# Performance work log

Hardware: AMD Instinct MI355X
Metric: run time of the kernel (lower is better)

Reference implementation:

```python
import jax, jax.numpy as jnp
import numpy as np

P = 14  # chain length, hard-coded by edge_index construction (range(14))
B = 4096
BN_EPS = 1e-5
ALPHA = 1.0
DIMS = [(3, 64), (64, 64), (64, 64), (64, 128), (128, 1024)]


def setup_inputs() -> dict:
    key = jax.random.key(0)
    ks = jax.random.split(key, 40)
    inp = {}
    inp["x1"] = jax.random.normal(ks[0], (B, 3, P), jnp.float32)
    inp["x2"] = jax.random.normal(ks[1], (B, 3, P), jnp.float32)
    for li, (din, dout) in enumerate(DIMS, 1):
        inp[f"W{li}"] = jax.random.normal(ks[1 + li], (din, dout), jnp.float32) / np.float32(np.sqrt(din))
        inp[f"b{li}"] = jnp.zeros((dout,), jnp.float32)
        inp[f"gamma{li}"] = jnp.ones((dout,), jnp.float32)
        inp[f"beta{li}"] = jnp.zeros((dout,), jnp.float32)
    inp["emb_W"] = jax.random.normal(ks[10], (1024, 10), jnp.float32) / np.float32(32.0)
    inp["emb_b"] = jnp.zeros((10,), jnp.float32)
    inp["clu_W"] = jax.random.normal(ks[11], (800, 10), jnp.float32) * np.float32(0.1)  # xavier-ish
    return inp


def _chain_agg(h):
    # h: [B*P, d]; equivalent to A @ h where A is the block-diagonal chain
    # adjacency (i<->i+1, no self-loops) built by the original Python loop.
    h3 = h.reshape(B, P, -1)
    agg = (jnp.pad(h3[:, 1:], ((0, 0), (0, 1), (0, 0)))
           + jnp.pad(h3[:, :-1], ((0, 0), (1, 0), (0, 0))))
    return agg.reshape(B * P, -1)


def _gcn_block(h, W, b, gamma, beta):
    # GCNConv: A @ (X W) + b ; then BatchNorm1d (training stats) ; ReLU
    h = _chain_agg(h @ W) + b
    mu = h.mean(axis=0)
    var = ((h - mu) ** 2).mean(axis=0)  # biased var, as torch BN uses for normalization
    h = gamma * (h - mu) * jax.lax.rsqrt(var + BN_EPS) + beta
    return jax.nn.relu(h)


def _forward_single(x, params):
    # x: [B, 3, P] -> [B, P, 3] -> [B*P, 3]
    h = jnp.transpose(x, (0, 2, 1)).reshape(B * P, 3)
    for li in range(1, 6):
        h = _gcn_block(h, params[f"W{li}"], params[f"b{li}"], params[f"gamma{li}"], params[f"beta{li}"])
    h = h.reshape(B, P, -1).max(axis=1)            # [B, 1024]
    extra = h @ params["emb_W"] + params["emb_b"]  # [B, 10]
    # ClusterlingLayer (Student-t assignment)
    d = jnp.sum((extra[:, None, :] - params["clu_W"]) ** 2, axis=2)  # [B, 800]
    q = (1.0 + d / ALPHA) ** (-(ALPHA + 1.0) / 2.0)
    q = q / q.sum(axis=1, keepdims=True)
    return q, extra, d


def reference(x1, x2, W1, b1, gamma1, beta1, W2, b2, gamma2, beta2,
              W3, b3, gamma3, beta3, W4, b4, gamma4, beta4,
              W5, b5, gamma5, beta5, emb_W, emb_b, clu_W):
    params = dict(W1=W1, b1=b1, gamma1=gamma1, beta1=beta1,
                  W2=W2, b2=b2, gamma2=gamma2, beta2=beta2,
                  W3=W3, b3=b3, gamma3=gamma3, beta3=beta3,
                  W4=W4, b4=b4, gamma4=gamma4, beta4=beta4,
                  W5=W5, b5=b5, gamma5=gamma5, beta5=beta5,
                  emb_W=emb_W, emb_b=emb_b, clu_W=clu_W)
    c1, e1, d1 = _forward_single(x1, params)
    c2, e2, d2 = _forward_single(x2, params)
    sim = jnp.linalg.norm(e1 - e2 + 1e-6, axis=1)  # torch pairwise_distance eps
    return sim, c1, c2, e1, e2, d1
```

## Files before the change

kernel.cpp:

```cpp
#include <hip/hip_runtime.h>
#include <hip/hip_bf16.h>

#define NB 4096
#define PLEN 14
#define NROWS (NB*PLEN)
#define BN_EPS 1e-5f

#define SLOT_STRIDE 32768
#define INP_STRIDE  133120
#define SLOT5_OFF   131072
#define NBANK 16

typedef __bf16 bf16x8 __attribute__((ext_vector_type(8)));
typedef float  f32x4  __attribute__((ext_vector_type(4)));

__global__ __launch_bounds__(256) void wprep_kernel(
    const float* __restrict__ W2, const float* __restrict__ W3,
    const float* __restrict__ W4, const float* __restrict__ W5,
    __bf16* __restrict__ wt2, __bf16* __restrict__ wt3,
    __bf16* __restrict__ wt4, __bf16* __restrict__ wt5b,
    float* __restrict__ stats)
{
    int idx = blockIdx.x*256 + threadIdx.x;
    if (idx < 2*INP_STRIDE) { stats[idx] = 0.f; return; }
    idx -= 2*INP_STRIDE;
    if (idx < 4096) { int n = idx>>6, k = idx&63; wt2[idx] = (__bf16)W2[k*64+n]; return; }
    idx -= 4096;
    if (idx < 4096) { int n = idx>>6, k = idx&63; wt3[idx] = (__bf16)W3[k*64+n]; return; }
    idx -= 4096;
    if (idx < 8192) { int n = idx>>6, k = idx&63; wt4[idx] = (__bf16)W4[k*128+n]; return; }
    idx -= 8192;
    int kk = idx & 7, n = (idx >> 3) & 63, kg = (idx >> 9) & 15, c = idx >> 13;
    wt5b[idx] = (__bf16)W5[(kg*8 + kk)*1024 + c*64 + n];
}

__global__ __launch_bounds__(256) void l1_kernel(
    const float* __restrict__ x1,
    const float* __restrict__ x2,
    const float* __restrict__ W,
    const float* __restrict__ bias,
    __bf16* __restrict__ pre,
    float* __restrict__ stats)
{
    const int col  = threadIdx.x & 63;
    const int sub  = threadIdx.x >> 6;
    const int chain = blockIdx.x * 4 + sub;
    const int inp  = chain >> 12;
    const int bank = blockIdx.x & (NBANK-1);
    const float w0 = W[0*64+col], w1 = W[1*64+col], w2 = W[2*64+col];
    const float bb = bias[col];
    const float* xb = (inp ? x2 : x1) + (chain & 4095)*3*PLEN;
    float s = 0.f, s2 = 0.f;
    for (int p = 0; p < PLEN; p++) {
        float u0 = 0.f, u1 = 0.f, u2 = 0.f;
        if (p > 0)      { u0 += xb[p-1]; u1 += xb[PLEN+p-1]; u2 += xb[2*PLEN+p-1]; }
        if (p < PLEN-1) { u0 += xb[p+1]; u1 += xb[PLEN+p+1]; u2 += xb[2*PLEN+p+1]; }
        float v = u0*w0 + u1*w1 + u2*w2 + bb;
        pre[(size_t)(chain*PLEN + p)*64 + col] = (__bf16)v;
        s += v; s2 += v*v;
    }
    __shared__ float ss[4][64], ssq[4][64];
    ss[sub][col] = s; ssq[sub][col] = s2;
    __syncthreads();
    if (sub == 0) {
        float ts  = ss[0][col]+ss[1][col]+ss[2][col]+ss[3][col];
        float ts2 = ssq[0][col]+ssq[1][col]+ssq[2][col]+ssq[3][col];
        float* st = stats + inp*INP_STRIDE + bank*2048;
        atomicAdd(&st[col], ts);
        atomicAdd(&st[1024 + col], ts2);
    }
}

template<int NOUT>
__global__ __launch_bounds__(256) void layer_kernel(
    const __bf16* __restrict__ prev,
    const float* __restrict__ stats_in,
    const float* __restrict__ gamma, const float* __restrict__ beta,
    const __bf16* __restrict__ wt,
    const float* __restrict__ bias,
    __bf16* __restrict__ outp,
    float* __restrict__ stats_out)
{
    constexpr int KP = 72;
    constexpr int NCH = NOUT/64;
    __shared__ __align__(16) short sA[64*KP];
    const int tid = threadIdx.x, wave = tid >> 6, lane = tid & 63;
    const int m = lane & 15, q = lane >> 4;
    const int rowbase = blockIdx.x * 56;
    const int soff = (blockIdx.x >> 10) * INP_STRIDE;
    const int bank = blockIdx.x & (NBANK-1);
    const float* sin_ = stats_in + soff;

    bf16x8 breg[NCH][2];
    #pragma unroll
    for (int cc = 0; cc < NCH; ++cc)
        #pragma unroll
        for (int ksi = 0; ksi < 2; ++ksi)
            breg[cc][ksi] = *reinterpret_cast<const bf16x8*>(
                wt + (cc*64 + wave*16 + m)*64 + ksi*32 + q*8);

    #pragma unroll
    for (int i = tid; i < 512; i += 256) {
        int rr = 56 + (i >> 6), cc = i & 63;
        sA[rr*KP + cc] = 0;
    }
    {
        const int ch = tid >> 6, c = tid & 63;
        float sb = 0.f, qb = 0.f;
        #pragma unroll
        for (int bk = 0; bk < NBANK; ++bk) {
            sb += sin_[bk*2048 + c];
            qb += sin_[bk*2048 + 1024 + c];
        }
        float mu = sb*(1.f/NROWS);
        float vr = qb*(1.f/NROWS) - mu*mu;
        float a = gamma[c]*rsqrtf(vr+BN_EPS), c0 = beta[c]-mu*a;
        float h[14];
        const __bf16* src = prev + (size_t)(rowbase + ch*14)*64 + c;
        #pragma unroll
        for (int r = 0; r < 14; ++r)
            h[r] = fmaxf(a*(float)src[r*64] + c0, 0.f);
        #pragma unroll
        for (int r = 0; r < 14; ++r) {
            float g = (r>0 ? h[r-1] : 0.f) + (r<13 ? h[r+1] : 0.f);
            union { __bf16 b; short s; } pk;
            pk.b = (__bf16)g;
            sA[(ch*14+r)*KP + c] = pk.s;
        }
    }
    __syncthreads();

    f32x4 acc[NCH][4];
    #pragma unroll
    for (int cc = 0; cc < NCH; ++cc)
        #pragma unroll
        for (int t = 0; t < 4; ++t) acc[cc][t] = (f32x4){0.f,0.f,0.f,0.f};

    #pragma unroll
    for (int ksi = 0; ksi < 2; ++ksi) {
        bf16x8 af[4];
        #pragma unroll
        for (int t = 0; t < 4; ++t)
            af[t] = *reinterpret_cast<const bf16x8*>(&sA[(t*16+m)*KP + ksi*32 + q*8]);
        #pragma unroll
        for (int cc = 0; cc < NCH; ++cc)
            #pragma unroll
            for (int t = 0; t < 4; ++t)
                acc[cc][t] = __builtin_amdgcn_mfma_f32_16x16x32_bf16(af[t], breg[cc][ksi], acc[cc][t], 0, 0, 0);
    }

    float* stout = stats_out + soff + bank*2048;
    #pragma unroll
    for (int cc = 0; cc < NCH; ++cc) {
        const int ocol = cc*64 + wave*16 + m;
        const float bb = bias[ocol];
        float s = 0.f, s2 = 0.f;
        #pragma unroll
        for (int t = 0; t < 4; ++t) {
            if (t == 3 && q >= 2) continue;
            #pragma unroll
            for (int r = 0; r < 4; ++r) {
                float v = acc[cc][t][r] + bb;
                outp[(size_t)(rowbase + t*16 + q*4 + r)*NOUT + ocol] = (__bf16)v;
                s += v; s2 += v*v;
            }
        }
        s  += __shfl_xor(s, 16);  s  += __shfl_xor(s, 32);
        s2 += __shfl_xor(s2, 16); s2 += __shfl_xor(s2, 32);
        if (lane < 16) {
            atomicAdd(&stout[ocol], s);
            atomicAdd(&stout[1024 + ocol], s2);
        }
    }
}

__global__ __launch_bounds__(256, 1) void l5_kernel(
    const __bf16* __restrict__ prev,
    const float* __restrict__ stats_in,
    const float* __restrict__ gamma, const float* __restrict__ beta,
    const __bf16* __restrict__ wtb,
    const float* __restrict__ bias,
    const float* __restrict__ g5,
    __bf16* __restrict__ osel,
    float* __restrict__ part)
{
    __shared__ __align__(16) short sA[112*136];
    const int tid = threadIdx.x, wave = tid >> 6, lane = tid & 63;
    const int m = lane & 15, q = lane >> 4;
    const int rowbase = blockIdx.x * 112;
    const int soff = (blockIdx.x >> 9) * INP_STRIDE;
    const float* sin_ = stats_in + soff;
    float* pb = part + (size_t)blockIdx.x * 2048;

    const char* gw = (const char*)wtb;
    const int boffB = q*1024 + (wave*16 + m)*16;

    bf16x8 bA[4], bB[4];
    #pragma unroll
    for (int k4 = 0; k4 < 4; ++k4)
        bA[k4] = *reinterpret_cast<const bf16x8*>(gw + boffB + k4*4096);

    {
        const int ch = tid >> 5, c4 = (tid & 31)*4;
        float aa[4], cc4[4];
        #pragma unroll
        for (int j = 0; j < 4; ++j) {
            float sb = 0.f, qb = 0.f;
            #pragma unroll
            for (int bk = 0; bk < NBANK; ++bk) {
                sb += sin_[bk*2048 + c4+j];
                qb += sin_[bk*2048 + 1024 + c4+j];
            }
            float mu = sb*(1.f/NROWS);
            float vr = qb*(1.f/NROWS) - mu*mu;
            aa[j] = gamma[c4+j]*rsqrtf(vr+BN_EPS);
            cc4[j] = beta[c4+j] - mu*aa[j];
        }
        float h[14][4];
        const __bf16* src = prev + (size_t)(rowbase + ch*14)*128 + c4;
        #pragma unroll
        for (int r = 0; r < 14; ++r) {
            union { uint2 u; __bf16 b[4]; } ld;
            ld.u = *reinterpret_cast<const uint2*>(src + r*128);
            h[r][0] = fmaxf(aa[0]*(float)ld.b[0] + cc4[0], 0.f);
            h[r][1] = fmaxf(aa[1]*(float)ld.b[1] + cc4[1], 0.f);
            h[r][2] = fmaxf(aa[2]*(float)ld.b[2] + cc4[2], 0.f);
            h[r][3] = fmaxf(aa[3]*(float)ld.b[3] + cc4[3], 0.f);
        }
        const int qq = ch >> 1, jb = (ch & 1) * 14;
        #pragma unroll
        for (int p = 0; p < 14; ++p) {
            int j = jb + p;
            int slot = (j>>2)*16 + qq*4 + (j&3);
            union { __bf16 b[4]; uint2 u; } pk;
            #pragma unroll
            for (int jj = 0; jj < 4; ++jj) {
                float g = (p>0 ? h[p-1][jj] : 0.f) + (p<13 ? h[p+1][jj] : 0.f);
                pk.b[jj] = (__bf16)g;
            }
            *reinterpret_cast<uint2*>(&sA[slot*136 + c4]) = pk.u;
        }
    }
    __syncthreads();

    bf16x8 af[7][4];
    #pragma unroll
    for (int t = 0; t < 7; ++t)
        #pragma unroll
        for (int kk = 0; kk < 4; ++kk)
            af[t][kk] = *reinterpret_cast<const bf16x8*>(&sA[(t*16 + m)*136 + kk*32 + q*8]);

    auto step = [&](int c, bf16x8 (&bR)[4]) {
        f32x4 acc[7];
        #pragma unroll
        for (int t = 0; t < 7; ++t) acc[t] = (f32x4){0.f,0.f,0.f,0.f};
        #pragma unroll
        for (int k4 = 0; k4 < 4; ++k4)
            #pragma unroll
            for (int t = 0; t < 7; ++t)
                acc[t] = __builtin_amdgcn_mfma_f32_16x16x32_bf16(af[t][k4], bR[k4], acc[t], 0, 0, 0);
        const int ocol = c*64 + wave*16 + m;
        const float bb = bias[ocol];
        const float sg = (g5[ocol] >= 0.f) ? 1.f : -1.f;
        float s = 0.f, s2 = 0.f;
        float mx0 = -3.4e38f, mx1 = -3.4e38f;
        #pragma unroll
        for (int t = 0; t < 7; ++t)
            #pragma unroll
            for (int r = 0; r < 4; ++r) {
                float v = acc[t][r] + bb;
                s += v; s2 += v*v;
                float va = sg * v;
                if (t*4 + r < 14) mx0 = fmaxf(mx0, va);
                else              mx1 = fmaxf(mx1, va);
            }
        osel[(size_t)(blockIdx.x*8 + 2*q    )*1024 + ocol] = (__bf16)(sg * mx0);
        osel[(size_t)(blockIdx.x*8 + 2*q + 1)*1024 + ocol] = (__bf16)(sg * mx1);
        s  += __shfl_xor(s, 16);  s  += __shfl_xor(s, 32);
        s2 += __shfl_xor(s2, 16); s2 += __shfl_xor(s2, 32);
        if (lane < 16) {
            pb[ocol]        = s;
            pb[1024 + ocol] = s2;
        }
    };

    #pragma unroll 1
    for (int cc = 0; cc < 16; cc += 2) {
        {
            const char* gb = gw + (size_t)(cc+1)*16384 + boffB;
            #pragma unroll
            for (int k4 = 0; k4 < 4; ++k4)
                bB[k4] = *reinterpret_cast<const bf16x8*>(gb + k4*4096);
        }
        step(cc, bA);
        if (cc + 2 < 16) {
            const char* gb = gw + (size_t)(cc+2)*16384 + boffB;
            #pragma unroll
            for (int k4 = 0; k4 < 4; ++k4)
                bA[k4] = *reinterpret_cast<const bf16x8*>(gb + k4*4096);
        }
        step(cc + 1, bB);
    }
}

__global__ __launch_bounds__(256) void sreduce_kernel(
    const float* __restrict__ part, float* __restrict__ stats)
{
    const int g = blockIdx.x*256 + threadIdx.x;
    const int slice = g >> 12;
    const int pair  = g & 4095;
    const int inp = pair >> 11;
    const int col = pair & 2047;
    const float* p = part + (size_t)inp*512*2048 + (size_t)slice*32*2048 + col;
    float s = 0.f;
    #pragma unroll 4
    for (int b = 0; b < 32; ++b)
        s += p[(size_t)b*2048];
    atomicAdd(&stats[inp*INP_STRIDE + SLOT5_OFF + col], s);
}

__global__ __launch_bounds__(256) void headclu_kernel(
    const __bf16* __restrict__ osel,
    const float* __restrict__ stats,
    const float* __restrict__ gamma, const float* __restrict__ beta,
    const float* __restrict__ embW, const float* __restrict__ embB,
    const float* __restrict__ cluW,
    float* __restrict__ e1, float* __restrict__ e2,
    float* __restrict__ c1, float* __restrict__ c2,
    float* __restrict__ d1, float* __restrict__ simOut)
{
    const int b = blockIdx.x, tid = threadIdx.x;
    const int wave = tid >> 6, lane = tid & 63;
    __shared__ float red[4][20];
    __shared__ float se[2][10];
    __shared__ float sred[4][2];

    const float* st0 = stats + SLOT5_OFF;
    const float* st1 = stats + INP_STRIDE + SLOT5_OFF;
    const __bf16* row0 = osel + (size_t)b*1024;
    const __bf16* row1 = osel + (size_t)(NB + b)*1024;

    float acc0[10], acc1[10];
    #pragma unroll
    for (int j = 0; j < 10; ++j) { acc0[j] = 0.f; acc1[j] = 0.f; }
    #pragma unroll
    for (int i = 0; i < 4; ++i) {
        int k = tid + i*256;
        float g = gamma[k], bt = beta[k];
        float mu0 = st0[k]*(1.f/NROWS);
        float va0 = st0[1024+k]*(1.f/NROWS) - mu0*mu0;
        float a0 = g*rsqrtf(va0+BN_EPS);
        float c0 = bt - mu0*a0;
        float mu1 = st1[k]*(1.f/NROWS);
        float va1 = st1[1024+k]*(1.f/NROWS) - mu1*mu1;
        float a1 = g*rsqrtf(va1+BN_EPS);
        float c1_ = bt - mu1*a1;
        float h0 = fmaxf(a0*(float)row0[k] + c0, 0.f);
        float h1 = fmaxf(a1*(float)row1[k] + c1_, 0.f);
        #pragma unroll
        for (int j = 0; j < 10; ++j) {
            float w = embW[k*10 + j];
            acc0[j] += h0 * w;
            acc1[j] += h1 * w;
        }
    }
    #pragma unroll
    for (int j = 0; j < 10; ++j) {
        acc0[j] += __shfl_down(acc0[j], 32);
        acc0[j] += __shfl_down(acc0[j], 16);
        acc0[j] += __shfl_down(acc0[j], 8);
        acc0[j] += __shfl_down(acc0[j], 4);
        acc0[j] += __shfl_down(acc0[j], 2);
        acc0[j] += __shfl_down(acc0[j], 1);
        acc1[j] += __shfl_down(acc1[j], 32);
        acc1[j] += __shfl_down(acc1[j], 16);
        acc1[j] += __shfl_down(acc1[j], 8);
        acc1[j] += __shfl_down(acc1[j], 4);
        acc1[j] += __shfl_down(acc1[j], 2);
        acc1[j] += __shfl_down(acc1[j], 1);
    }
    if (lane == 0)
        #pragma unroll
        for (int j = 0; j < 10; ++j) {
            red[wave][j]      = acc0[j];
            red[wave][10 + j] = acc1[j];
        }
    __syncthreads();
    if (tid < 20) {
        int inp = tid / 10, j = tid % 10;
        float t = red[0][tid]+red[1][tid]+red[2][tid]+red[3][tid] + embB[j];
        se[inp][j] = t;
        (inp ? e2 : e1)[b*10 + j] = t;
    }
    __syncthreads();

    float ev0[10], ev1[10];
    #pragma unroll
    for (int j = 0; j < 10; ++j) { ev0[j] = se[0][j]; ev1[j] = se[1][j]; }
    float d0loc[4], d1loc[4], q0loc[4], q1loc[4], qs0 = 0.f, qs1 = 0.f;
    #pragma unroll
    for (int i = 0; i < 4; ++i) {
        int mm = tid + i*256;
        float dd0 = 0.f, dd1 = 0.f;
        if (mm < 800) {
            #pragma unroll
            for (int j = 0; j < 10; ++j) {
                float cw = cluW[mm*10 + j];
                float t0 = ev0[j] - cw; dd0 += t0*t0;
                float t1 = ev1[j] - cw; dd1 += t1*t1;
            }
        }
        d0loc[i] = dd0; d1loc[i] = dd1;
        float q0v = (mm < 800) ? 1.f/(1.f + dd0) : 0.f;
        float q1v = (mm < 800) ? 1.f/(1.f + dd1) : 0.f;
        q0loc[i] = q0v; q1loc[i] = q1v;
        qs0 += q0v; qs1 += q1v;
    }
    float t0 = qs0, t1 = qs1;
    t0 += __shfl_down(t0,32); t0 += __shfl_down(t0,16); t0 += __shfl_down(t0,8);
    t0 += __shfl_down(t0,4);  t0 += __shfl_down(t0,2);  t0 += __shfl_down(t0,1);
    t1 += __shfl_down(t1,32); t1 += __shfl_down(t1,16); t1 += __shfl_down(t1,8);
    t1 += __shfl_down(t1,4);  t1 += __shfl_down(t1,2);  t1 += __shfl_down(t1,1);
    if (lane == 0) { sred[wave][0] = t0; sred[wave][1] = t1; }
    __syncthreads();
    float inv0 = 1.f / (sred[0][0]+sred[1][0]+sred[2][0]+sred[3][0]);
    float inv1 = 1.f / (sred[0][1]+sred[1][1]+sred[2][1]+sred[3][1]);
    #pragma unroll
    for (int i = 0; i < 4; ++i) {
        int mm = tid + i*256;
        if (mm < 800) {
            c1[(size_t)b*800 + mm] = q0loc[i]*inv0;
            c2[(size_t)b*800 + mm] = q1loc[i]*inv1;
            d1[(size_t)b*800 + mm] = d0loc[i];
        }
    }
    if (tid == 0) {
        float ss = 0.f;
        #pragma unroll
        for (int j = 0; j < 10; ++j) {
            float df = ev0[j] - ev1[j] + 1e-6f;
            ss += df*df;
        }
        simOut[b] = sqrtf(ss);
    }
}

extern "C" void kernel_launch(void* const* d_in, const int* in_sizes, int n_in,
                              void* d_out, int out_size, void* d_ws, size_t ws_size,
                              hipStream_t stream)
{
    const float* x1 = (const float*)d_in[0];
    const float* x2 = (const float*)d_in[1];
    const float *W[5], *bi[5], *ga[5], *be[5];
    for (int l = 0; l < 5; l++) {
        W[l]  = (const float*)d_in[2 + 4*l];
        bi[l] = (const float*)d_in[3 + 4*l];
        ga[l] = (const float*)d_in[4 + 4*l];
        be[l] = (const float*)d_in[5 + 4*l];
    }
    const float* embW = (const float*)d_in[22];
    const float* embB = (const float*)d_in[23];
    const float* cluW = (const float*)d_in[24];
    float* out = (float*)d_out;
    float* ws  = (float*)d_ws;

    float*  stats = ws;
    __bf16* wt2   = (__bf16*)(ws + 2*INP_STRIDE);
    __bf16* wt3   = wt2 + 4096;
    __bf16* wt4   = wt2 + 8192;
    __bf16* wt5b  = wt2 + 16384;
    float*  R1f   = ws + 2*INP_STRIDE + 73728;
    float*  R2f   = R1f + 8388608;
    __bf16* P0    = (__bf16*)R1f;
    __bf16* P1    = (__bf16*)R2f;
    __bf16* Q     = (__bf16*)R2f;
    __bf16* osel  = (__bf16*)R1f;
    float*  part  = R2f + 7340032;

    wprep_kernel<<<1616, 256, 0, stream>>>(W[1], W[2], W[3], W[4],
                                           wt2, wt3, wt4, wt5b, stats);

    float* simO = out;
    float* c1O  = out + 4096;
    float* c2O  = out + 3280896;
    float* e1O  = out + 6557696;
    float* e2O  = out + 6598656;
    float* d1O  = out + 6639616;

    l1_kernel<<<2048, 256, 0, stream>>>(x1, x2, W[0], bi[0], P0, stats);
    layer_kernel<64><<<2048, 256, 0, stream>>>(
        P0, stats + 0*SLOT_STRIDE, ga[0], be[0], wt2, bi[1], P1, stats + 1*SLOT_STRIDE);
    layer_kernel<64><<<2048, 256, 0, stream>>>(
        P1, stats + 1*SLOT_STRIDE, ga[1], be[1], wt3, bi[2], P0, stats + 2*SLOT_STRIDE);
    layer_kernel<128><<<2048, 256, 0, stream>>>(
        P0, stats + 2*SLOT_STRIDE, ga[2], be[2], wt4, bi[3], Q, stats + 3*SLOT_STRIDE);
    l5_kernel<<<1024, 256, 0, stream>>>(
        Q, stats + 3*SLOT_STRIDE, ga[3], be[3], wt5b, bi[4], ga[4], osel, part);
    sreduce_kernel<<<256, 256, 0, stream>>>(part, stats);
    headclu_kernel<<<4096, 256, 0, stream>>>(
        osel, stats, ga[4], be[4], embW, embB, cluW,
        e1O, e2O, c1O, c2O, d1O, simO);
}
```

Measured before the change: 249.9 us.

## Halve l5 tile to 4 samples per block and double grid size

The layer-5 kernel now handles 4 samples (56 rows padded to 64) per block instead of 8 (112 rows), and launches twice as many blocks. The smaller tile uses 4 MFMA row tiles instead of 7 and needs fewer accumulators and A fragments, so register pressure drops and more blocks are available to fill the GPU. In exchange, each block reloads the full W5 weights for half as much work, there are twice as many partial-stat rows for sreduce to sum, and padding rows must be zeroed. The sreduce indexing is updated to match the new partial count.

New measurement: 256.7 us. 2.7% more time.

```diff
diff --git a/kernel.cpp b/kernel.cpp
--- a/kernel.cpp
+++ b/kernel.cpp
@@ -184,11 +184,11 @@
     __bf16* __restrict__ osel,
     float* __restrict__ part)
 {
-    __shared__ __align__(16) short sA[112*136];
+    __shared__ __align__(16) short sA[64*136];
     const int tid = threadIdx.x, wave = tid >> 6, lane = tid & 63;
     const int m = lane & 15, q = lane >> 4;
-    const int rowbase = blockIdx.x * 112;
-    const int soff = (blockIdx.x >> 9) * INP_STRIDE;
+    const int rowbase = blockIdx.x * 56;
+    const int soff = (blockIdx.x >> 10) * INP_STRIDE;
     const float* sin_ = stats_in + soff;
     float* pb = part + (size_t)blockIdx.x * 2048;
 
@@ -200,82 +200,78 @@
     for (int k4 = 0; k4 < 4; ++k4)
         bA[k4] = *reinterpret_cast<const bf16x8*>(gw + boffB + k4*4096);
 
+    #pragma unroll
+    for (int i = tid; i < 1024; i += 256) {
+        int idx = i >> 7;
+        int row = 50 + (idx >> 1)*4 + (idx & 1);
+        sA[row*136 + (i & 127)] = 0;
+    }
     {
-        const int ch = tid >> 5, c4 = (tid & 31)*4;
-        float aa[4], cc4[4];
-        #pragma unroll
-        for (int j = 0; j < 4; ++j) {
+        const int ch = tid >> 6, c2 = (tid & 63)*2;
+        float aa[2], cc2[2];
+        #pragma unroll
+        for (int j = 0; j < 2; ++j) {
             float sb = 0.f, qb = 0.f;
             #pragma unroll
             for (int bk = 0; bk < NBANK; ++bk) {
-                sb += sin_[bk*2048 + c4+j];
-                qb += sin_[bk*2048 + 1024 + c4+j];
+                sb += sin_[bk*2048 + c2+j];
+                qb += sin_[bk*2048 + 1024 + c2+j];
             }
             float mu = sb*(1.f/NROWS);
             float vr = qb*(1.f/NROWS) - mu*mu;
-            aa[j] = gamma[c4+j]*rsqrtf(vr+BN_EPS);
-            cc4[j] = beta[c4+j] - mu*aa[j];
-        }
-        float h[14][4];
-        const __bf16* src = prev + (size_t)(rowbase + ch*14)*128 + c4;
+            aa[j] = gamma[c2+j]*rsqrtf(vr+BN_EPS);
+            cc2[j] = beta[c2+j] - mu*aa[j];
+        }
+        float h[14][2];
+        const __bf16* src = prev + (size_t)(rowbase + ch*14)*128 + c2;
         #pragma unroll
         for (int r = 0; r < 14; ++r) {
-            union { uint2 u; __bf16 b[4]; } ld;
-            ld.u = *reinterpret_cast<const uint2*>(src + r*128);
-            h[r][0] = fmaxf(aa[0]*(float)ld.b[0] + cc4[0], 0.f);
-            h[r][1] = fmaxf(aa[1]*(float)ld.b[1] + cc4[1], 0.f);
-            h[r][2] = fmaxf(aa[2]*(float)ld.b[2] + cc4[2], 0.f);
-            h[r][3] = fmaxf(aa[3]*(float)ld.b[3] + cc4[3], 0.f);
-        }
-        const int qq = ch >> 1, jb = (ch & 1) * 14;
+            union { unsigned u; __bf16 b[2]; } ld;
+            ld.u = *reinterpret_cast<const unsigned*>(src + r*128);
+            h[r][0] = fmaxf(aa[0]*(float)ld.b[0] + cc2[0], 0.f);
+            h[r][1] = fmaxf(aa[1]*(float)ld.b[1] + cc2[1], 0.f);
+        }
         #pragma unroll
         for (int p = 0; p < 14; ++p) {
-            int j = jb + p;
-            int slot = (j>>2)*16 + qq*4 + (j&3);
-            union { __bf16 b[4]; uint2 u; } pk;
-            #pragma unroll
-            for (int jj = 0; jj < 4; ++jj) {
-                float g = (p>0 ? h[p-1][jj] : 0.f) + (p<13 ? h[p+1][jj] : 0.f);
-                pk.b[jj] = (__bf16)g;
-            }
-            *reinterpret_cast<uint2*>(&sA[slot*136 + c4]) = pk.u;
-        }
-    }
-    __syncthreads();
-
-    bf16x8 af[7][4];
-    #pragma unroll
-    for (int t = 0; t < 7; ++t)
+            int slot = (p>>2)*16 + ch*4 + (p&3);
+            union { __bf16 b[2]; unsigned u; } pk;
+            pk.b[0] = (__bf16)((p>0 ? h[p-1][0] : 0.f) + (p<13 ? h[p+1][0] : 0.f));
+            pk.b[1] = (__bf16)((p>0 ? h[p-1][1] : 0.f) + (p<13 ? h[p+1][1] : 0.f));
+            *reinterpret_cast<unsigned*>(&sA[slot*136 + c2]) = pk.u;
+        }
+    }
+    __syncthreads();
+
+    bf16x8 af[4][4];
+    #pragma unroll
+    for (int t = 0; t < 4; ++t)
         #pragma unroll
         for (int kk = 0; kk < 4; ++kk)
             af[t][kk] = *reinterpret_cast<const bf16x8*>(&sA[(t*16 + m)*136 + kk*32 + q*8]);
 
     auto step = [&](int c, bf16x8 (&bR)[4]) {
-        f32x4 acc[7];
-        #pragma unroll
-        for (int t = 0; t < 7; ++t) acc[t] = (f32x4){0.f,0.f,0.f,0.f};
+        f32x4 acc[4];
+        #pragma unroll
+        for (int t = 0; t < 4; ++t) acc[t] = (f32x4){0.f,0.f,0.f,0.f};
         #pragma unroll
         for (int k4 = 0; k4 < 4; ++k4)
             #pragma unroll
-            for (int t = 0; t < 7; ++t)
+            for (int t = 0; t < 4; ++t)
                 acc[t] = __builtin_amdgcn_mfma_f32_16x16x32_bf16(af[t][k4], bR[k4], acc[t], 0, 0, 0);
         const int ocol = c*64 + wave*16 + m;
         const float bb = bias[ocol];
         const float sg = (g5[ocol] >= 0.f) ? 1.f : -1.f;
-        float s = 0.f, s2 = 0.f;
-        float mx0 = -3.4e38f, mx1 = -3.4e38f;
-        #pragma unroll
-        for (int t = 0; t < 7; ++t)
+        float s = 0.f, s2 = 0.f, mx = -3.4e38f;
+        #pragma unroll
+        for (int t = 0; t < 4; ++t)
             #pragma unroll
             for (int r = 0; r < 4; ++r) {
+                if (t*4 + r >= 14) continue;
                 float v = acc[t][r] + bb;
                 s += v; s2 += v*v;
-                float va = sg * v;
-                if (t*4 + r < 14) mx0 = fmaxf(mx0, va);
-                else              mx1 = fmaxf(mx1, va);
+                mx = fmaxf(mx, sg * v);
             }
-        osel[(size_t)(blockIdx.x*8 + 2*q    )*1024 + ocol] = (__bf16)(sg * mx0);
-        osel[(size_t)(blockIdx.x*8 + 2*q + 1)*1024 + ocol] = (__bf16)(sg * mx1);
+        osel[(size_t)(blockIdx.x*4 + q)*1024 + ocol] = (__bf16)(sg * mx);
         s  += __shfl_xor(s, 16);  s  += __shfl_xor(s, 32);
         s2 += __shfl_xor(s2, 16); s2 += __shfl_xor(s2, 32);
         if (lane < 16) {
@@ -311,10 +307,10 @@
     const int pair  = g & 4095;
     const int inp = pair >> 11;
     const int col = pair & 2047;
-    const float* p = part + (size_t)inp*512*2048 + (size_t)slice*32*2048 + col;
+    const float* p = part + (size_t)inp*1024*2048 + (size_t)slice*64*2048 + col;
     float s = 0.f;
     #pragma unroll 4
-    for (int b = 0; b < 32; ++b)
+    for (int b = 0; b < 64; ++b)
         s += p[(size_t)b*2048];
     atomicAdd(&stats[inp*INP_STRIDE + SLOT5_OFF + col], s);
 }
@@ -494,7 +490,7 @@
         P1, stats + 1*SLOT_STRIDE, ga[1], be[1], wt3, bi[2], P0, stats + 2*SLOT_STRIDE);
     layer_kernel<128><<<2048, 256, 0, stream>>>(
         P0, stats + 2*SLOT_STRIDE, ga[2], be[2], wt4, bi[3], Q, stats + 3*SLOT_STRIDE);
-    l5_kernel<<<1024, 256, 0, stream>>>(
+    l5_kernel<<<2048, 256, 0, stream>>>(
         Q, stats + 3*SLOT_STRIDE, ga[3], be[3], wt5b, bi[4], ga[4], osel, part);
     sreduce_kernel<<<256, 256, 0, stream>>>(part, stats);
     headclu_kernel<<<4096, 256, 0, stream>>>(
```
